# Optimization experiments

Hardware: AMD Instinct MI355X
Metric: run time of the kernel (lower is better)

The kernel has to match this reference:

```python
import jax, jax.numpy as jnp
import numpy as np

N, E, G = 128000, 2048000, 512
IN, ED, H, C = 12, 2, 64, 10
BN_EPS = 1e-5


def setup_inputs() -> dict:
    key = jax.random.key(0)
    ks = jax.random.split(key, 24)
    p = lambda k, s: (jax.random.normal(k, s, jnp.float32) * 0.05)
    inp = {
        "x": jax.random.normal(ks[0], (N, IN), jnp.float32),
        "edge_index": jax.random.randint(ks[1], (2, E), 0, N),
        "edge_attr": jax.random.normal(ks[2], (E, ED), jnp.float32),
        "batch": jnp.sort(jax.random.randint(ks[3], (N,), 0, G)),
        # edge encoders
        "We1": p(ks[4], (ED, IN)), "be1": jnp.zeros((IN,), jnp.float32),
        "We2": p(ks[5], (ED, H)), "be2": jnp.zeros((H,), jnp.float32),
        "We3": p(ks[6], (ED, H)), "be3": jnp.zeros((H,), jnp.float32),
        # GINE MLPs (Linear + BN eval-mode params)
        "W1": p(ks[7], (IN, H)), "b1": jnp.zeros((H,), jnp.float32),
        "g1": jnp.ones((H,), jnp.float32), "bt1": jnp.zeros((H,), jnp.float32),
        "rm1": jnp.zeros((H,), jnp.float32), "rv1": jnp.ones((H,), jnp.float32),
        "W2": p(ks[8], (H, H)), "b2": jnp.zeros((H,), jnp.float32),
        "g2": jnp.ones((H,), jnp.float32), "bt2": jnp.zeros((H,), jnp.float32),
        "rm2": jnp.zeros((H,), jnp.float32), "rv2": jnp.ones((H,), jnp.float32),
        "W3": p(ks[9], (H, H)), "b3": jnp.zeros((H,), jnp.float32),
        "g3": jnp.ones((H,), jnp.float32), "bt3": jnp.zeros((H,), jnp.float32),
        "rm3": jnp.zeros((H,), jnp.float32), "rv3": jnp.ones((H,), jnp.float32),
        # residual projection
        "Wr": p(ks[10], (IN, H)), "br": jnp.zeros((H,), jnp.float32),
        # classifier
        "Wc1": p(ks[11], (2 * H, H)), "bc1": jnp.zeros((H,), jnp.float32),
        "Wc2": p(ks[12], (H, C)), "bc2": jnp.zeros((C,), jnp.float32),
    }
    return inp


def _bn(h, g, b, rm, rv):
    return g * (h - rm) * jax.lax.rsqrt(rv + BN_EPS) + b


def _gine(x, src, dst, e_emb, W, b, g, bt, rm, rv):
    # message = ReLU(x_j + edge_emb), scatter-sum at target; eps = 0
    msg = jax.nn.relu(x[src] + e_emb)                       # [E, d]
    agg = jax.ops.segment_sum(msg, dst, num_segments=x.shape[0])
    return jax.nn.relu(_bn((x + agg) @ W + b, g, bt, rm, rv))


def reference(x, edge_index, edge_attr, batch,
              We1, be1, We2, be2, We3, be3,
              W1, b1, g1, bt1, rm1, rv1,
              W2, b2, g2, bt2, rm2, rv2,
              W3, b3, g3, bt3, rm3, rv3,
              Wr, br, Wc1, bc1, Wc2, bc2):
    src, dst = edge_index[0], edge_index[1]
    # eval mode: dropout is identity, BN uses running stats
    h = _gine(x, src, dst, edge_attr @ We1 + be1, W1, b1, g1, bt1, rm1, rv1) + (x @ Wr + br)
    h = _gine(h, src, dst, edge_attr @ We2 + be2, W2, b2, g2, bt2, rm2, rv2) + h
    h = _gine(h, src, dst, edge_attr @ We3 + be3, W3, b3, g3, bt3, rm3, rv3) + h
    counts = jax.ops.segment_sum(jnp.ones((h.shape[0],), h.dtype), batch, num_segments=G)
    mean = jax.ops.segment_sum(h, batch, num_segments=G) / jnp.maximum(counts, 1.0)[:, None]
    mx = jax.ops.segment_max(h, batch, num_segments=G)
    mx = jnp.where(counts[:, None] > 0, mx, 0.0)
    pooled = jnp.concatenate([mean, mx], axis=1)            # [G, 2H]
    return jax.nn.relu(pooled @ Wc1 + bc1) @ Wc2 + bc2      # [G, C]
```

## Files before the change

kernel.cpp:

```cpp
#include <hip/hip_runtime.h>
#include <hip/hip_bf16.h>
#include <hip/hip_fp16.h>

#define N_NODES 128000
#define E_EDGES 2048000
#define G_GRAPHS 512
#define D_IN 12
#define D_H 64
#define N_CLS 10
#define BN_EPS 1e-5f
#define NB 1000
#define BCAP 2560
#define TILE 8192
#define NPW 8
#define NPW12 4

typedef _Float16 h2vec __attribute__((ext_vector_type(2)));
typedef _Float16 h4vec __attribute__((ext_vector_type(4)));

__device__ __forceinline__ unsigned char f32_to_fp8(float v) {
    return (unsigned char)(__builtin_amdgcn_cvt_pk_fp8_f32(v, v, 0, false) & 0xff);
}


__global__ __launch_bounds__(256) void k_bin(const int* __restrict__ src, const int* __restrict__ dst,
                                             const float2* __restrict__ attr, int* __restrict__ gcount,
                                             int2* __restrict__ stage) {
    __shared__ int hist[NB];
    __shared__ int base_s[NB];
    __shared__ int rk[TILE];
    const int t = threadIdx.x;
    const int e0 = blockIdx.x * TILE;
    for (int i = t; i < NB; i += 256) hist[i] = 0;
    __syncthreads();
    for (int i = t; i < TILE; i += 256) {
        int d = dst[e0 + i];
        int b = d >> 7;
        int r = atomicAdd(&hist[b], 1);
        rk[i] = (b << 20) | ((d & 127) << 13) | r;
    }
    __syncthreads();
    for (int i = t; i < NB; i += 256) {
        int cb = hist[i];
        base_s[i] = i * BCAP + ((cb > 0) ? atomicAdd(&gcount[i], cb) : 0);
    }
    __syncthreads();
    for (int i = t; i < TILE; i += 256) {
        int pr = rk[i];
        int b = pr >> 20, dl = (pr >> 13) & 127, r = pr & 8191;
        float2 a = attr[e0 + i];
        __half2 h2 = __floats2half2_rn(a.x, a.y);
        stage[base_s[b] + r] = make_int2(src[e0 + i] | (dl << 17), *(int*)&h2);
    }
}

__global__ __launch_bounds__(256) void k_bscan(const int* __restrict__ gcount, int* __restrict__ bbase,
                                               int* __restrict__ offsets) {
    __shared__ int sm[256];
    const int t = threadIdx.x;
    int c0 = gcount[t * 4], c1 = gcount[t * 4 + 1], c2 = gcount[t * 4 + 2], c3 = gcount[t * 4 + 3];
    int s = c0 + c1 + c2 + c3;
    sm[t] = s;
    __syncthreads();
    for (int off = 1; off < 256; off <<= 1) {
        int x = 0;
        if (t >= off) x = sm[t - off];
        __syncthreads();
        sm[t] += x;
        __syncthreads();
    }
    int base = sm[t] - s;
    if (t * 4 < NB)     bbase[t * 4]     = base;
    if (t * 4 + 1 < NB) bbase[t * 4 + 1] = base + c0;
    if (t * 4 + 2 < NB) bbase[t * 4 + 2] = base + c0 + c1;
    if (t * 4 + 3 < NB) bbase[t * 4 + 3] = base + c0 + c1 + c2;
    if (t == 255) offsets[N_NODES] = sm[255];
}

__global__ __launch_bounds__(256) void k_final(const int* __restrict__ gcount, const int* __restrict__ bbase,
                                               const int2* __restrict__ stage,
                                               int* __restrict__ offsets, int2* __restrict__ edges) {
    __shared__ int2 recs[BCAP];
    __shared__ int cnt[128];
    __shared__ int incl[128];
    const int b = blockIdx.x, t = threadIdx.x;
    const int count = gcount[b];
    const int base = bbase[b];
    if (t < 128) cnt[t] = 0;
    __syncthreads();
    for (int i = t; i < count; i += 256) {
        int2 r = stage[b * BCAP + i];
        recs[i] = r;
        atomicAdd(&cnt[(r.x >> 17) & 127], 1);
    }
    __syncthreads();
    if (t < 128) incl[t] = cnt[t];
    __syncthreads();
    for (int off = 1; off < 128; off <<= 1) {
        int x = 0;
        if (t >= off && t < 128) x = incl[t - off];
        __syncthreads();
        if (t < 128) incl[t] += x;
        __syncthreads();
    }
    if (t < 128) {
        int ex = incl[t] - cnt[t];
        offsets[b * 128 + t] = base + ex;
        cnt[t] = ex;
    }
    __syncthreads();
    for (int i = t; i < count; i += 256) {
        int2 r = recs[i];
        int dl = (r.x >> 17) & 127;
        int p = atomicAdd(&cnt[dl], 1);
        edges[base + p] = make_int2(r.x & 0x1FFFF, r.y);
    }
}

__global__ __launch_bounds__(256) void k_pack_x(const float* __restrict__ x, __half* __restrict__ x16) {
    int idx = blockIdx.x * 256 + threadIdx.x;
    if (idx >= (N_NODES + 1) * 16) return;
    int n = idx >> 4, ch = idx & 15;
    float v = (n == N_NODES) ? -30000.f : ((ch < D_IN) ? x[n * D_IN + ch] : 0.f);
    x16[idx] = __float2half(v);
}

__global__ __launch_bounds__(256) void k_gine12(
    const float* __restrict__ x, const __half* __restrict__ x16,
    __half* __restrict__ hout, unsigned char* __restrict__ hout8,
    const int* __restrict__ off, const int2* __restrict__ edges,
    const float* __restrict__ We1, const float* __restrict__ be1,
    const float* __restrict__ W1, const float* __restrict__ b1,
    const float* __restrict__ g1, const float* __restrict__ bt1,
    const float* __restrict__ rm1, const float* __restrict__ rv1,
    const float* __restrict__ Wr, const float* __restrict__ br) {
    __shared__ float W1lds[D_IN * 64];
    __shared__ float Wrlds[D_IN * 64];
    __shared__ float uacc[4][16];
    __shared__ float u_lds[4][D_IN];
    __shared__ float x_lds[4][D_IN];
    const int t = threadIdx.x, w = t >> 6, c = t & 63;
    const int asb = (c >> 3) << 2;
    const int dwoff = (c & 7) << 2;
    const int ch0 = (c & 7) << 1;
    for (int i = t; i < D_IN * 64; i += 256) {
        W1lds[i] = W1[i];
        Wrlds[i] = Wr[i];
    }
    h2vec wp0 = {(_Float16)0.f, (_Float16)0.f}, wp1 = wp0;
    float bp0 = 0.f, bp1 = 0.f;
    if (ch0 < D_IN)     { wp0[0] = (_Float16)We1[ch0];     wp0[1] = (_Float16)We1[D_IN + ch0];     bp0 = be1[ch0]; }
    if (ch0 + 1 < D_IN) { wp1[0] = (_Float16)We1[ch0 + 1]; wp1[1] = (_Float16)We1[D_IN + ch0 + 1]; bp1 = be1[ch0 + 1]; }
    const float sj = g1[c] * rsqrtf(rv1[c] + BN_EPS);
    const float cj = (b1[c] - rm1[c]) * sj + bt1[c];
    const float brj = br[c];
    __syncthreads();

    const int wbase = (blockIdx.x * 4 + w) * NPW12;
    for (int nn = 0; nn < NPW12; ++nn) {
        const int n = wbase + nn;
        const int rs = off[n], re = off[n + 1];
        float a0 = 0.f, a1 = 0.f;
        for (int base = rs; base < re; base += 64) {
            const int cnt = min(64, re - base);
            int2 rec = make_int2(N_NODES, 0);
            if (c < cnt) rec = edges[base + c];
            for (int j0 = 0; j0 < cnt; j0 += 16) {
                const int ab = (j0 << 2) + asb;
                int s0 = __builtin_amdgcn_ds_bpermute(ab,      rec.x);
                int s1 = __builtin_amdgcn_ds_bpermute(ab + 32, rec.x);
                int e0 = __builtin_amdgcn_ds_bpermute(ab,      rec.y);
                int e1 = __builtin_amdgcn_ds_bpermute(ab + 32, rec.y);
                int ld0 = *(const int*)((const char*)x16 + ((s0 << 5) + dwoff));
                int ld1 = *(const int*)((const char*)x16 + ((s1 << 5) + dwoff));
                {
                    h2vec hv = __builtin_bit_cast(h2vec, ld0);
                    h2vec av = __builtin_bit_cast(h2vec, e0);
                    float q0 = __builtin_amdgcn_fdot2(av, wp0, bp0, false);
                    float q1 = __builtin_amdgcn_fdot2(av, wp1, bp1, false);
                    a0 += fmaxf((float)hv[0] + q0, 0.f);
                    a1 += fmaxf((float)hv[1] + q1, 0.f);
                }
                {
                    h2vec hv = __builtin_bit_cast(h2vec, ld1);
                    h2vec av = __builtin_bit_cast(h2vec, e1);
                    float q0 = __builtin_amdgcn_fdot2(av, wp0, bp0, false);
                    float q1 = __builtin_amdgcn_fdot2(av, wp1, bp1, false);
                    a0 += fmaxf((float)hv[0] + q0, 0.f);
                    a1 += fmaxf((float)hv[1] + q1, 0.f);
                }
            }
        }
        a0 += __shfl_xor(a0, 8);  a1 += __shfl_xor(a1, 8);
        a0 += __shfl_xor(a0, 16); a1 += __shfl_xor(a1, 16);
        a0 += __shfl_xor(a0, 32); a1 += __shfl_xor(a1, 32);
        uacc[w][ch0] = a0;
        uacc[w][ch0 + 1] = a1;
        if (c < D_IN) {
            float xc = x[(size_t)n * D_IN + c];
            x_lds[w][c] = xc;
            u_lds[w][c] = xc + uacc[w][c];
        }
        float z = 0.f, r = 0.f;
#pragma unroll
        for (int k = 0; k < D_IN; ++k) {
            z = fmaf(u_lds[w][k], W1lds[k * 64 + c], z);
            r = fmaf(x_lds[w][k], Wrlds[k * 64 + c], r);
        }
        float v = fmaxf(fmaf(z, sj, cj), 0.f) + r + brj;
        hout[(size_t)n * 64 + c] = __float2half(v);
        hout8[(size_t)n * 64 + c] = f32_to_fp8(v);
    }
}

__global__ __launch_bounds__(256) void k_gine64(
    const __half* __restrict__ hin, const unsigned char* __restrict__ hin8,
    __half* __restrict__ hout, unsigned char* __restrict__ hout8,
    const int* __restrict__ off, const int2* __restrict__ edges,
    const float* __restrict__ We, const float* __restrict__ be,
    const float* __restrict__ W, const float* __restrict__ b,
    const float* __restrict__ g, const float* __restrict__ bt,
    const float* __restrict__ rm, const float* __restrict__ rv) {
    __shared__ _Float16 WtL[64][68];
    __shared__ _Float16 uL[4][64];
    const int t = threadIdx.x, w = t >> 6, c = t & 63;
    for (int i = t; i < 4096; i += 256) {
        int k = i >> 6, cc = i & 63;
        WtL[cc][k] = (_Float16)W[i];
    }
    const int asb   = (c >> 4) << 2;
    const int dwoff = (c & 15) << 2;
    const int q4    = (c & 15) << 2;
    h2vec weq[4];
    float beq[4];
#pragma unroll
    for (int j = 0; j < 4; ++j) {
        weq[j][0] = (_Float16)We[q4 + j];
        weq[j][1] = (_Float16)We[64 + q4 + j];
        beq[j] = be[q4 + j];
    }
    const float sj = g[c] * rsqrtf(rv[c] + BN_EPS);
    const float cj = (b[c] - rm[c]) * sj + bt[c];
    __syncthreads();

    const int wbase = (blockIdx.x * 4 + w) * NPW;

    int offv[NPW + 1];
#pragma unroll
    for (int i = 0; i <= NPW; ++i) offv[i] = off[wbase + i];

    int2 rec0[NPW];
#pragma unroll
    for (int i = 0; i < NPW; ++i) {
        int2 r = make_int2(N_NODES, 0);
        if (c < offv[i + 1] - offv[i]) r = edges[offv[i] + c];
        rec0[i] = r;
    }
    float hcv[NPW];
#pragma unroll
    for (int i = 0; i < NPW; ++i) hcv[i] = __half2float(hin[(size_t)(wbase + i) * 64 + c]);

    int ldA[NPW * 4], eyA[NPW * 4];
#pragma unroll
    for (int i = 0; i < NPW; ++i) {
#pragma unroll
        for (int j = 0; j < 4; ++j) {
            int sx = __builtin_amdgcn_ds_bpermute(asb + (j << 4), rec0[i].x);
            eyA[i * 4 + j] = __builtin_amdgcn_ds_bpermute(asb + (j << 4), rec0[i].y);
            ldA[i * 4 + j] = *(const int*)(hin8 + ((sx << 6) + dwoff));
        }
    }

#define CONSUME(LD, EA)                                                          \
    {                                                                            \
        h2vec av = __builtin_bit_cast(h2vec, EA);                                \
        float q0 = __builtin_amdgcn_fdot2(av, weq[0], beq[0], false);            \
        float q1 = __builtin_amdgcn_fdot2(av, weq[1], beq[1], false);            \
        float q2 = __builtin_amdgcn_fdot2(av, weq[2], beq[2], false);            \
        float q3 = __builtin_amdgcn_fdot2(av, weq[3], beq[3], false);            \
        acc0 += fmaxf(__builtin_amdgcn_cvt_f32_fp8(LD, 0) + q0, 0.f);            \
        acc1 += fmaxf(__builtin_amdgcn_cvt_f32_fp8(LD, 1) + q1, 0.f);            \
        acc2 += fmaxf(__builtin_amdgcn_cvt_f32_fp8(LD, 2) + q2, 0.f);            \
        acc3 += fmaxf(__builtin_amdgcn_cvt_f32_fp8(LD, 3) + q3, 0.f);            \
    }

#pragma unroll
    for (int nn = 0; nn < NPW; ++nn) {
        const int n = wbase + nn;
        const int rs = offv[nn], re = offv[nn + 1];
        const float hc = hcv[nn];
        float acc0 = 0.f, acc1 = 0.f, acc2 = 0.f, acc3 = 0.f;
        CONSUME(ldA[nn * 4 + 0], eyA[nn * 4 + 0])
        CONSUME(ldA[nn * 4 + 1], eyA[nn * 4 + 1])
        CONSUME(ldA[nn * 4 + 2], eyA[nn * 4 + 2])
        CONSUME(ldA[nn * 4 + 3], eyA[nn * 4 + 3])
        const int cnt0 = min(64, re - rs);
        for (int j0 = 16; j0 < cnt0; j0 += 16) {
            const int ab = (j0 << 2) + asb;
            int s0 = __builtin_amdgcn_ds_bpermute(ab,      rec0[nn].x);
            int s1 = __builtin_amdgcn_ds_bpermute(ab + 16, rec0[nn].x);
            int s2 = __builtin_amdgcn_ds_bpermute(ab + 32, rec0[nn].x);
            int s3 = __builtin_amdgcn_ds_bpermute(ab + 48, rec0[nn].x);
            int e0 = __builtin_amdgcn_ds_bpermute(ab,      rec0[nn].y);
            int e1 = __builtin_amdgcn_ds_bpermute(ab + 16, rec0[nn].y);
            int e2 = __builtin_amdgcn_ds_bpermute(ab + 32, rec0[nn].y);
            int e3 = __builtin_amdgcn_ds_bpermute(ab + 48, rec0[nn].y);
            int ld0 = *(const int*)(hin8 + ((s0 << 6) + dwoff));
            int ld1 = *(const int*)(hin8 + ((s1 << 6) + dwoff));
            int ld2 = *(const int*)(hin8 + ((s2 << 6) + dwoff));
            int ld3 = *(const int*)(hin8 + ((s3 << 6) + dwoff));
            CONSUME(ld0, e0)
            CONSUME(ld1, e1)
            CONSUME(ld2, e2)
            CONSUME(ld3, e3)
        }
        for (int base = rs + 64; base < re; base += 64) {
            const int cnt = min(64, re - base);
            int2 rec = make_int2(N_NODES, 0);
            if (c < cnt) rec = edges[base + c];
            for (int j0 = 0; j0 < cnt; j0 += 16) {
                const int ab = (j0 << 2) + asb;
                int s0 = __builtin_amdgcn_ds_bpermute(ab,      rec.x);
                int s1 = __builtin_amdgcn_ds_bpermute(ab + 16, rec.x);
                int s2 = __builtin_amdgcn_ds_bpermute(ab + 32, rec.x);
                int s3 = __builtin_amdgcn_ds_bpermute(ab + 48, rec.x);
                int e0 = __builtin_amdgcn_ds_bpermute(ab,      rec.y);
                int e1 = __builtin_amdgcn_ds_bpermute(ab + 16, rec.y);
                int e2 = __builtin_amdgcn_ds_bpermute(ab + 32, rec.y);
                int e3 = __builtin_amdgcn_ds_bpermute(ab + 48, rec.y);
                int ld0 = *(const int*)(hin8 + ((s0 << 6) + dwoff));
                int ld1 = *(const int*)(hin8 + ((s1 << 6) + dwoff));
                int ld2 = *(const int*)(hin8 + ((s2 << 6) + dwoff));
                int ld3 = *(const int*)(hin8 + ((s3 << 6) + dwoff));
                CONSUME(ld0, e0)
                CONSUME(ld1, e1)
                CONSUME(ld2, e2)
                CONSUME(ld3, e3)
            }
        }
        acc0 += __shfl_xor(acc0, 16); acc1 += __shfl_xor(acc1, 16);
        acc2 += __shfl_xor(acc2, 16); acc3 += __shfl_xor(acc3, 16);
        acc0 += __shfl_xor(acc0, 32); acc1 += __shfl_xor(acc1, 32);
        acc2 += __shfl_xor(acc2, 32); acc3 += __shfl_xor(acc3, 32);
        h4vec aq = {(_Float16)acc0, (_Float16)acc1, (_Float16)acc2, (_Float16)acc3};
        *(h4vec*)&uL[w][q4] = aq;
        float u = hc + (float)uL[w][c];
        uL[w][c] = (_Float16)u;
        float z = 0.f;
        const h4vec* u4p = (const h4vec*)uL[w];
        const h4vec* wt4p = (const h4vec*)&WtL[c][0];
#pragma unroll
        for (int k4 = 0; k4 < 16; ++k4) {
            h4vec uu = u4p[k4];
            h4vec ww = wt4p[k4];
            h2vec ul = __builtin_shufflevector(uu, uu, 0, 1);
            h2vec uh = __builtin_shufflevector(uu, uu, 2, 3);
            h2vec wl = __builtin_shufflevector(ww, ww, 0, 1);
            h2vec wh = __builtin_shufflevector(ww, ww, 2, 3);
            z = __builtin_amdgcn_fdot2(ul, wl, z, false);
            z = __builtin_amdgcn_fdot2(uh, wh, z, false);
        }
        float v = fmaxf(fmaf(z, sj, cj), 0.f) + hc;
        hout[(size_t)n * 64 + c] = __float2half(v);
        hout8[(size_t)n * 64 + c] = f32_to_fp8(v);
    }
#undef CONSUME
}

__global__ __launch_bounds__(256) void k_pool(
    const __half* __restrict__ h, const int* __restrict__ batch,
    const float* __restrict__ Wc1, const float* __restrict__ bc1,
    const float* __restrict__ Wc2, const float* __restrict__ bc2,
    float* __restrict__ out) {
    __shared__ float psum[4][64];
    __shared__ float pmax[4][64];
    __shared__ float pool[128];
    __shared__ float hid[64];
    const int t = threadIdx.x, w = t >> 6, c = t & 63;
    const int g = blockIdx.x;
    int lo = 0, hi = N_NODES;
    while (lo < hi) { int mid = (lo + hi) >> 1; if (batch[mid] < g) lo = mid + 1; else hi = mid; }
    int start = lo;
    hi = N_NODES;
    while (lo < hi) { int mid = (lo + hi) >> 1; if (batch[mid] < g + 1) lo = mid + 1; else hi = mid; }
    int end = lo;

    float s = 0.f, m = -3.4e38f;
    for (int i = start + w; i < end; i += 4) {
        float v = __half2float(h[(size_t)i * 64 + c]);
        s += v;
        m = fmaxf(m, v);
    }
    psum[w][c] = s;
    pmax[w][c] = m;
    __syncthreads();
    if (w == 0) {
        float ss = psum[0][c] + psum[1][c] + psum[2][c] + psum[3][c];
        float mm = fmaxf(fmaxf(pmax[0][c], pmax[1][c]), fmaxf(pmax[2][c], pmax[3][c]));
        int cnt = end - start;
        pool[c] = ss / fmaxf((float)cnt, 1.f);
        pool[64 + c] = (cnt > 0) ? mm : 0.f;
    }
    __syncthreads();
    if (t < 64) {
        float z = bc1[t];
#pragma unroll 8
        for (int k = 0; k < 128; ++k) z = fmaf(pool[k], Wc1[k * 64 + t], z);
        hid[t] = fmaxf(z, 0.f);
    }
    __syncthreads();
    if (t < N_CLS) {
        float z = bc2[t];
#pragma unroll
        for (int k = 0; k < 64; ++k) z = fmaf(hid[k], Wc2[k * N_CLS + t], z);
        out[g * N_CLS + t] = z;
    }
}

extern "C" void kernel_launch(void* const* d_in, const int* in_sizes, int n_in,
                              void* d_out, int out_size, void* d_ws, size_t ws_size,
                              hipStream_t stream) {
    const float* x     = (const float*)d_in[0];
    const int*   ei    = (const int*)d_in[1];
    const float* ea    = (const float*)d_in[2];
    const int*   batch = (const int*)d_in[3];
    const float* We1 = (const float*)d_in[4],  *be1 = (const float*)d_in[5];
    const float* We2 = (const float*)d_in[6],  *be2 = (const float*)d_in[7];
    const float* We3 = (const float*)d_in[8],  *be3 = (const float*)d_in[9];
    const float* W1 = (const float*)d_in[10], *b1 = (const float*)d_in[11];
    const float* g1 = (const float*)d_in[12], *bt1 = (const float*)d_in[13];
    const float* rm1 = (const float*)d_in[14], *rv1 = (const float*)d_in[15];
    const float* W2 = (const float*)d_in[16], *b2 = (const float*)d_in[17];
    const float* g2 = (const float*)d_in[18], *bt2 = (const float*)d_in[19];
    const float* rm2 = (const float*)d_in[20], *rv2 = (const float*)d_in[21];
    const float* W3 = (const float*)d_in[22], *b3 = (const float*)d_in[23];
    const float* g3 = (const float*)d_in[24], *bt3 = (const float*)d_in[25];
    const float* rm3 = (const float*)d_in[26], *rv3 = (const float*)d_in[27];
    const float* Wr = (const float*)d_in[28], *br = (const float*)d_in[29];
    const float* Wc1 = (const float*)d_in[30], *bc1 = (const float*)d_in[31];
    const float* Wc2 = (const float*)d_in[32], *bc2 = (const float*)d_in[33];

    int* off    = (int*)d_ws;
    int* gcount = off + (N_NODES + 4);
    int* bbase  = gcount + 1024;
    int2* edges = (int2*)(bbase + 1024);
    int2* stage = edges + E_EDGES;
    __half* hA  = (__half*)(stage + (size_t)NB * BCAP);
    __half* hB  = hA + (size_t)N_NODES * 64;
    unsigned char* hA8 = (unsigned char*)(hB + (size_t)N_NODES * 64);
    unsigned char* hB8 = hA8 + (size_t)(N_NODES + 1) * 64;
    __half* x16 = (__half*)(hB8 + (size_t)(N_NODES + 1) * 64);

    hipMemsetAsync(gcount, 0, 1024 * sizeof(int), stream);
    hipMemsetAsync(hA8 + (size_t)N_NODES * 64, 0xFE, 64, stream);
    hipMemsetAsync(hB8 + (size_t)N_NODES * 64, 0xFE, 64, stream);

    const int* src = ei;
    const int* dst = ei + E_EDGES;

    k_pack_x<<<((N_NODES + 1) * 16 + 255) / 256, 256, 0, stream>>>(x, x16);
    k_bin<<<E_EDGES / TILE, 256, 0, stream>>>(src, dst, (const float2*)ea, gcount, stage);
    k_bscan<<<1, 256, 0, stream>>>(gcount, bbase, off);
    k_final<<<NB, 256, 0, stream>>>(gcount, bbase, stage, off, edges);

    k_gine12<<<N_NODES / (4 * NPW12), 256, 0, stream>>>(x, x16, hA, hA8, off, edges,
                                                        We1, be1, W1, b1, g1, bt1, rm1, rv1, Wr, br);
    const int g64_blocks = N_NODES / (4 * NPW);
    k_gine64<<<g64_blocks, 256, 0, stream>>>(hA, hA8, hB, hB8, off, edges,
                                             We2, be2, W2, b2, g2, bt2, rm2, rv2);
    k_gine64<<<g64_blocks, 256, 0, stream>>>(hB, hB8, hA, hA8, off, edges,
                                             We3, be3, W3, b3, g3, bt3, rm3, rv3);
    k_pool<<<G_GRAPHS, 256, 0, stream>>>(hA, batch, Wc1, bc1, Wc2, bc2, (float*)d_out);
}
```

Baseline: 454.8 us.

## Sort binned edges in shared memory and double-buffer gather prefetch in GINE kernel

In the binning kernel, edges within a tile are first placed into bucket order in shared memory via a block-wide prefix scan over the histogram. Consecutive threads then write to contiguous staging slots, which should improve write coalescing at the cost of extra LDS and sync passes. In the aggregation kernel, the up-front prefetch of all 8 nodes' first gathers is replaced with a two-slot ping-pong that issues the next node's gathers while consuming the current one. This reduces register pressure, which may raise occupancy, but leaves less memory latency hidden per node.

```diff
diff --git a/kernel.cpp b/kernel.cpp
--- a/kernel.cpp
+++ b/kernel.cpp
@@ -28,7 +28,10 @@
                                              int2* __restrict__ stage) {
     __shared__ int hist[NB];
     __shared__ int base_s[NB];
+    __shared__ int bscan[NB];
     __shared__ int rk[TILE];
+    __shared__ unsigned short sorted[TILE];
+    __shared__ int psum[256];
     const int t = threadIdx.x;
     const int e0 = blockIdx.x * TILE;
     for (int i = t; i < NB; i += 256) hist[i] = 0;
@@ -40,12 +43,38 @@
         rk[i] = (b << 20) | ((d & 127) << 13) | r;
     }
     __syncthreads();
+    int h0 = (t * 4     < NB) ? hist[t * 4]     : 0;
+    int h1 = (t * 4 + 1 < NB) ? hist[t * 4 + 1] : 0;
+    int h2 = (t * 4 + 2 < NB) ? hist[t * 4 + 2] : 0;
+    int h3 = (t * 4 + 3 < NB) ? hist[t * 4 + 3] : 0;
+    int s = h0 + h1 + h2 + h3;
+    psum[t] = s;
+    __syncthreads();
+    for (int off = 1; off < 256; off <<= 1) {
+        int x = 0;
+        if (t >= off) x = psum[t - off];
+        __syncthreads();
+        psum[t] += x;
+        __syncthreads();
+    }
+    int base = psum[t] - s;
+    if (t * 4     < NB) bscan[t * 4]     = base;
+    if (t * 4 + 1 < NB) bscan[t * 4 + 1] = base + h0;
+    if (t * 4 + 2 < NB) bscan[t * 4 + 2] = base + h0 + h1;
+    if (t * 4 + 3 < NB) bscan[t * 4 + 3] = base + h0 + h1 + h2;
     for (int i = t; i < NB; i += 256) {
         int cb = hist[i];
         base_s[i] = i * BCAP + ((cb > 0) ? atomicAdd(&gcount[i], cb) : 0);
     }
     __syncthreads();
     for (int i = t; i < TILE; i += 256) {
+        int pr = rk[i];
+        int b = pr >> 20, r = pr & 8191;
+        sorted[bscan[b] + r] = (unsigned short)i;
+    }
+    __syncthreads();
+    for (int p = t; p < TILE; p += 256) {
+        int i = sorted[p];
         int pr = rk[i];
         int b = pr >> 20, dl = (pr >> 13) & 127, r = pr & 8191;
         float2 a = attr[e0 + i];
@@ -256,21 +285,17 @@
         if (c < offv[i + 1] - offv[i]) r = edges[offv[i] + c];
         rec0[i] = r;
     }
-    float hcv[NPW];
-#pragma unroll
-    for (int i = 0; i < NPW; ++i) hcv[i] = __half2float(hin[(size_t)(wbase + i) * 64 + c]);
-
-    int ldA[NPW * 4], eyA[NPW * 4];
-#pragma unroll
-    for (int i = 0; i < NPW; ++i) {
-#pragma unroll
-        for (int j = 0; j < 4; ++j) {
-            int sx = __builtin_amdgcn_ds_bpermute(asb + (j << 4), rec0[i].x);
-            eyA[i * 4 + j] = __builtin_amdgcn_ds_bpermute(asb + (j << 4), rec0[i].y);
-            ldA[i * 4 + j] = *(const int*)(hin8 + ((sx << 6) + dwoff));
-        }
-    }
-
+
+    int ldP[2][4], eyP[2][4];
+#define ISSUE(P, I)                                                              \
+    {                                                                            \
+        _Pragma("unroll")                                                        \
+        for (int j = 0; j < 4; ++j) {                                            \
+            int sx = __builtin_amdgcn_ds_bpermute(asb + (j << 4), rec0[I].x);    \
+            eyP[P][j] = __builtin_amdgcn_ds_bpermute(asb + (j << 4), rec0[I].y); \
+            ldP[P][j] = *(const int*)(hin8 + ((sx << 6) + dwoff));               \
+        }                                                                        \
+    }
 #define CONSUME(LD, EA)                                                          \
     {                                                                            \
         h2vec av = __builtin_bit_cast(h2vec, EA);                                \
@@ -284,16 +309,19 @@
         acc3 += fmaxf(__builtin_amdgcn_cvt_f32_fp8(LD, 3) + q3, 0.f);            \
     }
 
+    ISSUE(0, 0)
 #pragma unroll
     for (int nn = 0; nn < NPW; ++nn) {
+        const int p = nn & 1;
+        if (nn + 1 < NPW) ISSUE(p ^ 1, nn + 1)
         const int n = wbase + nn;
         const int rs = offv[nn], re = offv[nn + 1];
-        const float hc = hcv[nn];
+        const float hc = __half2float(hin[(size_t)n * 64 + c]);
         float acc0 = 0.f, acc1 = 0.f, acc2 = 0.f, acc3 = 0.f;
-        CONSUME(ldA[nn * 4 + 0], eyA[nn * 4 + 0])
-        CONSUME(ldA[nn * 4 + 1], eyA[nn * 4 + 1])
-        CONSUME(ldA[nn * 4 + 2], eyA[nn * 4 + 2])
-        CONSUME(ldA[nn * 4 + 3], eyA[nn * 4 + 3])
+        CONSUME(ldP[p][0], eyP[p][0])
+        CONSUME(ldP[p][1], eyP[p][1])
+        CONSUME(ldP[p][2], eyP[p][2])
+        CONSUME(ldP[p][3], eyP[p][3])
         const int cnt0 = min(64, re - rs);
         for (int j0 = 16; j0 < cnt0; j0 += 16) {
             const int ab = (j0 << 2) + asb;
@@ -365,6 +393,7 @@
         hout8[(size_t)n * 64 + c] = f32_to_fp8(v);
     }
 #undef CONSUME
+#undef ISSUE
 }
 
 __global__ __launch_bounds__(256) void k_pool(
```

Result: faster. 430.0 us (-5.4%).
